# Kernel optimization log

Measured on AMD Instinct MI355X. Metric: run time of the kernel, lower is better.

Reference implementation:

```python
import jax, jax.numpy as jnp
import numpy as np

B, C, S, H, W = 2, 192, 16, 32, 32
NH, P = 6, 4          # num_heads, n_points (n_points hardcoded = 4 in source)
HD = C // NH          # head_dim = 32
HID = 4 * C           # mlp hidden (mlp_ratio = 4.0)
L = S * H * W
EPS = 1e-5


def _offset_bias():
    # Faithful to DeformAttention._reset_parameters grid init.
    thetas = np.arange(NH, dtype=np.float32) * (2.0 * np.pi / NH)
    g = np.stack([np.cos(thetas), np.sin(thetas) * np.cos(thetas), np.sin(thetas) * np.sin(thetas)], -1)
    g = g / np.abs(g).max(-1, keepdims=True)
    g = np.tile(g[:, None, :], (1, P, 1)).copy()
    for i in range(P):
        g[:, i, :] *= (i + 1)
    return jnp.asarray(g.reshape(-1), dtype=jnp.float32)


def setup_inputs() -> dict:
    key = jax.random.key(0)
    ks = jax.random.split(key, 8)
    w = lambda k, shp, s: jax.random.normal(k, shp, jnp.float32) * s
    return {
        "x": jax.random.normal(ks[0], (B, C, S, H, W), jnp.float32),
        "mask_matrix": 0,  # unused (shift_size == 0)
        "Wv": w(ks[1], (C, C), C ** -0.5), "bv": jnp.zeros((C,), jnp.float32),
        "Woff": w(ks[2], (C, NH * P * 3), 0.01), "boff": _offset_bias(),
        "Waw": w(ks[3], (C, NH * P), 0.02), "baw": jnp.zeros((NH * P,), jnp.float32),
        "Wout": w(ks[4], (C, C), C ** -0.5), "bout": jnp.zeros((C,), jnp.float32),
        "g2": jnp.ones((C,), jnp.float32), "b2": jnp.zeros((C,), jnp.float32),
        "W1": w(ks[5], (C, HID), C ** -0.5), "b1": jnp.zeros((HID,), jnp.float32),
        "W2": w(ks[6], (HID, C), HID ** -0.5), "b2m": jnp.zeros((C,), jnp.float32),
    }


def _layernorm(x, g, b):
    m = jnp.mean(x, -1, keepdims=True)
    v = jnp.mean(jnp.square(x - m), -1, keepdims=True)
    return (x - m) * jax.lax.rsqrt(v + EPS) * g + b


def _ref_points():
    # get_reference_points with valid_ratios == 1 (mask_ is all-zeros in source).
    d = (jnp.arange(S, dtype=jnp.float32) + 0.5) / S
    y = (jnp.arange(H, dtype=jnp.float32) + 0.5) / H
    x = (jnp.arange(W, dtype=jnp.float32) + 0.5) / W
    rd, ry, rx = jnp.meshgrid(d, y, x, indexing="ij")
    # stacked as (d, x, y), matching normalizer (D, W, H)
    return jnp.stack([rd.reshape(-1), rx.reshape(-1), ry.reshape(-1)], -1)  # (L, 3)


def _deform_core(value, loc, aw):
    # value: (B,L,NH,HD); loc: (B,L,NH,P,3) in [0,1] as (d,x,y); aw: (B,L,NH,P)
    v = value.transpose(0, 2, 1, 3)  # (B,NH,L,HD), L flattened as d*H*W + y*W + x
    pd = loc[..., 0] * S - 0.5  # align_corners=False pixel coords
    px = loc[..., 1] * W - 0.5
    py = loc[..., 2] * H - 0.5
    d0f, x0f, y0f = jnp.floor(pd), jnp.floor(px), jnp.floor(py)
    fd, fx, fy = pd - d0f, px - x0f, py - y0f
    d0, x0, y0 = d0f.astype(jnp.int32), x0f.astype(jnp.int32), y0f.astype(jnp.int32)
    acc = jnp.zeros((B, NH, L * P, HD), value.dtype)
    for dd in (0, 1):
        for dy in (0, 1):
            for dx in (0, 1):
                di, yi, xi = d0 + dd, y0 + dy, x0 + dx
                wgt = (fd if dd else 1.0 - fd) * (fy if dy else 1.0 - fy) * (fx if dx else 1.0 - fx)
                inb = (di >= 0) & (di < S) & (yi >= 0) & (yi < H) & (xi >= 0) & (xi < W)
                idx = (jnp.clip(di, 0, S - 1) * H + jnp.clip(yi, 0, H - 1)) * W + jnp.clip(xi, 0, W - 1)
                idx = idx.transpose(0, 2, 1, 3).reshape(B, NH, L * P)
                samp = jnp.take_along_axis(v, idx[..., None], axis=2)  # (B,NH,L*P,HD)
                wz = jnp.where(inb, wgt, 0.0).transpose(0, 2, 1, 3).reshape(B, NH, L * P, 1)
                acc = acc + samp * wz
    acc = acc.reshape(B, NH, L, P, HD)
    out = jnp.sum(acc * aw.transpose(0, 2, 1, 3)[..., None], axis=3)  # (B,NH,L,HD)
    return out.transpose(0, 2, 1, 3).reshape(B, L, NH * HD)


def reference(x, mask_matrix, Wv, bv, Woff, boff, Waw, baw, Wout, bout, g2, b2, W1, b1, W2, b2m):
    # shortcut = x.view(B, S*H*W, C) on channel-first memory (faithful to source view)
    shortcut = x.reshape(B, L, C)
    xp = x.transpose(0, 2, 3, 4, 1).reshape(B, L, C)  # token-major layout used by attn

    # DeformAttention
    value = (xp @ Wv + bv).reshape(B, L, NH, HD)
    off = (xp @ Woff + boff).reshape(B, L, NH, P, 3)
    aw = jax.nn.softmax((xp @ Waw + baw).reshape(B, L, NH, P), axis=-1)
    norm = jnp.array([S, W, H], jnp.float32)
    loc = _ref_points()[None, :, None, None, :] + off / norm  # (B,L,NH,P,3)
    attn = _deform_core(value, loc, aw) @ Wout + bout  # (B,L,C)

    h = shortcut + attn
    h = h + (jax.nn.gelu(_layernorm(h, g2, b2) @ W1 + b1, approximate=False) @ W2 + b2m)
    return h.reshape(B, S, H, W, C).transpose(0, 4, 1, 2, 3)  # (B,C,S,H,W)
```

## Files before the change

kernel.cpp:

```cpp
#include <hip/hip_runtime.h>
#include <hip/hip_bf16.h>
#include <math.h>

#define BB 2
#define CC 192
#define SS 16
#define HH 32
#define WW 32
#define NH 6
#define PP 4
#define HD 32
#define HID 768
#define LL (SS * HH * WW)
#define MTOK (BB * LL)
#define NPROJ 288

typedef unsigned short u16;
typedef u16 u16x8 __attribute__((ext_vector_type(8)));
typedef __bf16 bf16x8 __attribute__((ext_vector_type(8)));
typedef float f32x4 __attribute__((ext_vector_type(4)));

static __device__ __forceinline__ u16 f2b(float f) {
    __hip_bfloat16 h = __float2bfloat16(f);
    return *reinterpret_cast<u16*>(&h);
}

static __device__ __forceinline__ float fast_gelu(float v) {
    float z = 1.5957691216057308f * (v + 0.044715f * v * v * v);
    return v * __builtin_amdgcn_rcpf(1.0f + __expf(-z));
}

__global__ void build_weights(const float* __restrict__ Wv, const float* __restrict__ Woff,
                              const float* __restrict__ Waw, const float* __restrict__ Wout,
                              const float* __restrict__ W1, const float* __restrict__ W2,
                              const float* __restrict__ bv, const float* __restrict__ boff,
                              const float* __restrict__ baw,
                              u16* __restrict__ wcatT, u16* __restrict__ woutT,
                              u16* __restrict__ w1T, u16* __restrict__ w2T,
                              float* __restrict__ bcat) {
    int i = blockIdx.x * 256 + threadIdx.x;
    if (i < NPROJ * CC) {
        int n = i / CC, k = i % CC;
        float v = (n < 192) ? Wv[k * 192 + n]
                : (n < 264) ? Woff[k * 72 + (n - 192)]
                            : Waw[k * 24 + (n - 264)];
        wcatT[i] = f2b(v);
        return;
    }
    i -= NPROJ * CC;
    if (i < CC * CC) {
        int n = i / CC, k = i % CC;
        woutT[i] = f2b(Wout[k * CC + n]);
        return;
    }
    i -= CC * CC;
    if (i < HID * CC) {
        int n = i / CC, k = i % CC;
        w1T[i] = f2b(W1[k * HID + n]);
        return;
    }
    i -= HID * CC;
    if (i < CC * HID) {
        int n = i / HID, k = i % HID;
        w2T[i] = f2b(W2[k * CC + n]);
        return;
    }
    i -= CC * HID;
    if (i < NPROJ) {
        float v = (i < 192) ? bv[i] : (i < 264) ? boff[i - 192] : baw[i - 264];
        bcat[i] = v;
    }
}

__global__ void transpose_in(const float* __restrict__ x, u16* __restrict__ xp) {
    __shared__ float s[32][33];
    int b = blockIdx.z;
    int c0 = blockIdx.y * 32;
    int l0 = blockIdx.x * 32;
    int tx = threadIdx.x, ty = threadIdx.y;
#pragma unroll
    for (int r = 0; r < 32; r += 8)
        s[ty + r][tx] = x[((size_t)b * CC + c0 + ty + r) * LL + l0 + tx];
    __syncthreads();
#pragma unroll
    for (int r = 0; r < 32; r += 8)
        xp[((size_t)b * LL + l0 + ty + r) * CC + c0 + tx] = f2b(s[tx][ty + r]);
}

template<int EPI, int NF>
__global__ __launch_bounds__(256, 2) void gemm_mfma(const u16* __restrict__ A,
                                                    const u16* __restrict__ Bt,
                                                    const float* __restrict__ bias,
                                                    const float* __restrict__ add,
                                                    void* __restrict__ Cout,
                                                    void* __restrict__ Cout2,
                                                    int M, int N, int K) {
    constexpr int BN = NF * 32;
    constexpr int NB = (BN * 4 + 255) / 256;
    __shared__ u16 As[2][128][40];
    __shared__ u16 Bs[2][BN][40];
    int t = threadIdx.x;
    int m0 = blockIdx.y * 128;
    int n0 = blockIdx.x * BN;
    int w = t >> 6, lane = t & 63;
    int wm = w >> 1, wn = w & 1;
    int lrow = lane & 15, q = lane >> 4;
    int lk8 = q * 8;

    f32x4 acc[4][NF];
#pragma unroll
    for (int i = 0; i < 4; ++i)
#pragma unroll
        for (int f = 0; f < NF; ++f)
#pragma unroll
            for (int r = 0; r < 4; ++r) acc[i][f][r] = 0.f;

    int arow = t >> 2, aseg = (t & 3) * 8;
    const u16* Arow0 = A + (size_t)(m0 + arow) * K + aseg;
    const u16* Arow1 = A + (size_t)(m0 + arow + 64) * K + aseg;

    u16x8 av0, av1, bv[NB];
    av0 = *reinterpret_cast<const u16x8*>(Arow0);
    av1 = *reinterpret_cast<const u16x8*>(Arow1);
#pragma unroll
    for (int u2 = 0; u2 < NB; ++u2) {
        int ii = t + u2 * 256;
        if (ii < BN * 4) {
            int br = ii >> 2, bseg = (ii & 3) * 8;
            bv[u2] = *reinterpret_cast<const u16x8*>(Bt + (size_t)(n0 + br) * K + bseg);
        }
    }
    *reinterpret_cast<u16x8*>(&As[0][arow][aseg]) = av0;
    *reinterpret_cast<u16x8*>(&As[0][arow + 64][aseg]) = av1;
#pragma unroll
    for (int u2 = 0; u2 < NB; ++u2) {
        int ii = t + u2 * 256;
        if (ii < BN * 4) {
            int br = ii >> 2, bseg = (ii & 3) * 8;
            *reinterpret_cast<u16x8*>(&Bs[0][br][bseg]) = bv[u2];
        }
    }
    __syncthreads();

    int NT = K >> 5;
    int cur = 0;
    for (int ti = 0; ti < NT - 1; ++ti) {
        int k1 = (ti + 1) << 5;
        av0 = *reinterpret_cast<const u16x8*>(Arow0 + k1);
        av1 = *reinterpret_cast<const u16x8*>(Arow1 + k1);
#pragma unroll
        for (int u2 = 0; u2 < NB; ++u2) {
            int ii = t + u2 * 256;
            if (ii < BN * 4) {
                int br = ii >> 2, bseg = (ii & 3) * 8;
                bv[u2] = *reinterpret_cast<const u16x8*>(Bt + (size_t)(n0 + br) * K + k1 + bseg);
            }
        }
        {
            bf16x8 af[4], bfr[NF];
#pragma unroll
            for (int i = 0; i < 4; ++i)
                af[i] = *reinterpret_cast<const bf16x8*>(&As[cur][wm * 64 + i * 16 + lrow][lk8]);
#pragma unroll
            for (int f = 0; f < NF; ++f)
                bfr[f] = *reinterpret_cast<const bf16x8*>(&Bs[cur][wn * (16 * NF) + f * 16 + lrow][lk8]);
#pragma unroll
            for (int i = 0; i < 4; ++i)
#pragma unroll
                for (int f = 0; f < NF; ++f) {
                    if (EPI == 3)
                        acc[i][f] = __builtin_amdgcn_mfma_f32_16x16x32_bf16(af[i], bfr[f], acc[i][f], 0, 0, 0);
                    else
                        acc[i][f] = __builtin_amdgcn_mfma_f32_16x16x32_bf16(bfr[f], af[i], acc[i][f], 0, 0, 0);
                }
        }
        *reinterpret_cast<u16x8*>(&As[cur ^ 1][arow][aseg]) = av0;
        *reinterpret_cast<u16x8*>(&As[cur ^ 1][arow + 64][aseg]) = av1;
#pragma unroll
        for (int u2 = 0; u2 < NB; ++u2) {
            int ii = t + u2 * 256;
            if (ii < BN * 4) {
                int br = ii >> 2, bseg = (ii & 3) * 8;
                *reinterpret_cast<u16x8*>(&Bs[cur ^ 1][br][bseg]) = bv[u2];
            }
        }
        __syncthreads();
        cur ^= 1;
    }
    {
        bf16x8 af[4], bfr[NF];
#pragma unroll
        for (int i = 0; i < 4; ++i)
            af[i] = *reinterpret_cast<const bf16x8*>(&As[cur][wm * 64 + i * 16 + lrow][lk8]);
#pragma unroll
        for (int f = 0; f < NF; ++f)
            bfr[f] = *reinterpret_cast<const bf16x8*>(&Bs[cur][wn * (16 * NF) + f * 16 + lrow][lk8]);
#pragma unroll
        for (int i = 0; i < 4; ++i)
#pragma unroll
            for (int f = 0; f < NF; ++f) {
                if (EPI == 3)
                    acc[i][f] = __builtin_amdgcn_mfma_f32_16x16x32_bf16(af[i], bfr[f], acc[i][f], 0, 0, 0);
                else
                    acc[i][f] = __builtin_amdgcn_mfma_f32_16x16x32_bf16(bfr[f], af[i], acc[i][f], 0, 0, 0);
            }
    }

    if (EPI == 3) {
#pragma unroll
        for (int i = 0; i < 4; ++i) {
#pragma unroll
            for (int f = 0; f < NF; ++f) {
                int n = n0 + wn * (16 * NF) + f * 16 + lrow;
                float bvn = bias[n];
                int mb = m0 + wm * 64 + i * 16 + q * 4;
                float4 vv;
#pragma unroll
                for (int r = 0; r < 4; ++r)
                    ((float*)&vv)[r] = acc[i][f][r] + bvn + add[(size_t)(mb + r) * N + n];
                int b = mb >> 14, l = mb & (LL - 1);
                *reinterpret_cast<float4*>((float*)Cout + ((size_t)b * CC + n) * LL + l) = vv;
            }
        }
    } else {
#pragma unroll
        for (int i = 0; i < 4; ++i) {
            int m = m0 + wm * 64 + i * 16 + lrow;
#pragma unroll
            for (int f = 0; f < NF; ++f) {
                int nq = n0 + wn * (16 * NF) + f * 16 + q * 4;
                float4 bias4 = *reinterpret_cast<const float4*>(bias + nq);
                if (EPI == 0) {
                    if (nq < 192) {
                        int h = nq >> 5, hd = nq & 31;
                        int b = m >> 14, l = m & (LL - 1);
                        u16 p0 = f2b(acc[i][f][0] + bias4.x);
                        u16 p1 = f2b(acc[i][f][1] + bias4.y);
                        u16 p2 = f2b(acc[i][f][2] + bias4.z);
                        u16 p3 = f2b(acc[i][f][3] + bias4.w);
                        uint2 pk = make_uint2((unsigned)p0 | ((unsigned)p1 << 16),
                                              (unsigned)p2 | ((unsigned)p3 << 16));
                        *reinterpret_cast<uint2*>(
                            (u16*)Cout + (((size_t)b * NH + h) * LL + l) * HD + hd) = pk;
                    } else {
                        float4 vv;
                        vv.x = acc[i][f][0] + bias4.x;
                        vv.y = acc[i][f][1] + bias4.y;
                        vv.z = acc[i][f][2] + bias4.z;
                        vv.w = acc[i][f][3] + bias4.w;
                        *reinterpret_cast<float4*>((float*)Cout2 + (size_t)m * 96 + (nq - 192)) = vv;
                    }
                } else if (EPI == 1) {
                    float4 add4 = *reinterpret_cast<const float4*>(add + (size_t)m * N + nq);
                    float4 vv;
                    vv.x = acc[i][f][0] + bias4.x + add4.x;
                    vv.y = acc[i][f][1] + bias4.y + add4.y;
                    vv.z = acc[i][f][2] + bias4.z + add4.z;
                    vv.w = acc[i][f][3] + bias4.w + add4.w;
                    *reinterpret_cast<float4*>((float*)Cout + (size_t)m * N + nq) = vv;
                } else {
                    u16 p0 = f2b(fast_gelu(acc[i][f][0] + bias4.x));
                    u16 p1 = f2b(fast_gelu(acc[i][f][1] + bias4.y));
                    u16 p2 = f2b(fast_gelu(acc[i][f][2] + bias4.z));
                    u16 p3 = f2b(fast_gelu(acc[i][f][3] + bias4.w));
                    uint2 pk = make_uint2((unsigned)p0 | ((unsigned)p1 << 16),
                                          (unsigned)p2 | ((unsigned)p3 << 16));
                    *reinterpret_cast<uint2*>((u16*)Cout + (size_t)m * N + nq) = pk;
                }
            }
        }
    }
}

__global__ __launch_bounds__(256) void deform_kernel(const u16* __restrict__ vbuf,
                                                     const float* __restrict__ offaw,
                                                     u16* __restrict__ dout) {
    __shared__ uint2 cw[8][32];
    int gl = threadIdx.x >> 5;
    int g = blockIdx.x * 8 + gl;
    int j = threadIdx.x & 31;
    int h = g % NH;
    int tmp = g / NH;
    int l = tmp % LL;
    int b = tmp / LL;
    int d = l >> 10, rem = l & 1023, y = rem >> 5, xw = rem & 31;

    const float* oa = offaw + (size_t)(b * LL + l) * 96;
    int p = j >> 3, cor = j & 7;
    int dx = cor & 1, dy = (cor >> 1) & 1, dd = cor >> 2;

    float4 lg = *reinterpret_cast<const float4*>(oa + 72 + h * 4);
    float mx = fmaxf(fmaxf(lg.x, lg.y), fmaxf(lg.z, lg.w));
    float e0 = __expf(lg.x - mx), e1 = __expf(lg.y - mx);
    float e2 = __expf(lg.z - mx), e3 = __expf(lg.w - mx);
    float inv = __builtin_amdgcn_rcpf(e0 + e1 + e2 + e3);
    float ep = (p == 0) ? e0 : (p == 1) ? e1 : (p == 2) ? e2 : e3;
    float awp = ep * inv;

    const float* op = oa + (h * 4 + p) * 3;
    float pd = (d + 0.5f) + op[0] - 0.5f;
    float px = (xw + 0.5f) + op[1] - 0.5f;
    float py = (y + 0.5f) + op[2] - 0.5f;
    float d0f = floorf(pd), x0f = floorf(px), y0f = floorf(py);
    float fd = pd - d0f, fx = px - x0f, fy = py - y0f;
    int di = (int)d0f + dd, yi = (int)y0f + dy, xi = (int)x0f + dx;
    bool inb = (di >= 0) & (di < SS) & (yi >= 0) & (yi < HH) & (xi >= 0) & (xi < WW);
    float wgt = (dd ? fd : 1.f - fd) * (dy ? fy : 1.f - fy) * (dx ? fx : 1.f - fx) * awp;
    wgt = inb ? wgt : 0.f;
    int dic = min(max(di, 0), SS - 1);
    int yic = min(max(yi, 0), HH - 1);
    int xic = min(max(xi, 0), WW - 1);
    int bo = (((dic * HH) + yic) * WW + xic) * (HD * 2);

    cw[gl][j] = make_uint2((unsigned)bo, __float_as_uint(wgt));
    __syncthreads();

    int half = j >> 4, jc = j & 15;
    const char* vbase2 = (const char*)(vbuf + ((size_t)(b * NH + h) * LL) * HD) + 4 * jc;
    const uint4* cw4 = reinterpret_cast<const uint4*>(&cw[gl][half * 16]);
    float a0 = 0.f, a1 = 0.f;
#pragma unroll
    for (int qq = 0; qq < 8; ++qq) {
        uint4 c = cw4[qq];
        unsigned u0 = *reinterpret_cast<const unsigned*>(vbase2 + c.x);
        unsigned u1 = *reinterpret_cast<const unsigned*>(vbase2 + c.z);
        float w0 = __uint_as_float(c.y), w1 = __uint_as_float(c.w);
        a0 += w0 * __uint_as_float(u0 << 16);
        a1 += w0 * __uint_as_float(u0 & 0xffff0000u);
        a0 += w1 * __uint_as_float(u1 << 16);
        a1 += w1 * __uint_as_float(u1 & 0xffff0000u);
    }
    a0 += __shfl_xor(a0, 16);
    a1 += __shfl_xor(a1, 16);
    if (half == 0) {
        unsigned pk = (unsigned)f2b(a0) | ((unsigned)f2b(a1) << 16);
        *reinterpret_cast<unsigned*>(dout + (size_t)(b * LL + l) * CC + h * HD + 2 * jc) = pk;
    }
}

__global__ __launch_bounds__(256) void layernorm_kernel(const float* __restrict__ hin,
                                                        const float* __restrict__ g2,
                                                        const float* __restrict__ b2,
                                                        u16* __restrict__ lnout) {
    int row = blockIdx.x * 4 + (threadIdx.x >> 6);
    int lane = threadIdx.x & 63;
    const float* hr = hin + (size_t)row * CC;
    float v0 = hr[lane], v1 = hr[lane + 64], v2 = hr[lane + 128];
    float s = v0 + v1 + v2;
    float sq = v0 * v0 + v1 * v1 + v2 * v2;
#pragma unroll
    for (int o = 32; o > 0; o >>= 1) {
        s += __shfl_xor(s, o);
        sq += __shfl_xor(sq, o);
    }
    float m = s * (1.0f / CC);
    float var = sq * (1.0f / CC) - m * m;
    float r = rsqrtf(var + 1e-5f);
    u16* lo = lnout + (size_t)row * CC;
    lo[lane]       = f2b((v0 - m) * r * g2[lane]       + b2[lane]);
    lo[lane + 64]  = f2b((v1 - m) * r * g2[lane + 64]  + b2[lane + 64]);
    lo[lane + 128] = f2b((v2 - m) * r * g2[lane + 128] + b2[lane + 128]);
}

extern "C" void kernel_launch(void* const* d_in, const int* in_sizes, int n_in,
                              void* d_out, int out_size, void* d_ws, size_t ws_size,
                              hipStream_t stream) {
    const float* x    = (const float*)d_in[0];
    const float* Wv   = (const float*)d_in[2];
    const float* bv   = (const float*)d_in[3];
    const float* Woff = (const float*)d_in[4];
    const float* boff = (const float*)d_in[5];
    const float* Waw  = (const float*)d_in[6];
    const float* baw  = (const float*)d_in[7];
    const float* Wout = (const float*)d_in[8];
    const float* bout = (const float*)d_in[9];
    const float* g2   = (const float*)d_in[10];
    const float* b2   = (const float*)d_in[11];
    const float* W1   = (const float*)d_in[12];
    const float* b1   = (const float*)d_in[13];
    const float* W2   = (const float*)d_in[14];
    const float* b2m  = (const float*)d_in[15];

    char* wsb = (char*)d_ws;
    u16*   xp    = (u16*)(wsb + 0);
    u16*   vbuf  = (u16*)(wsb + 12582912);
    float* offaw = (float*)(wsb + 25165824);
    u16*   dbuf  = (u16*)(wsb + 0);
    u16*   hid   = (u16*)(wsb + 12582912);
    float* hbuf  = (float*)(wsb + 66060288);
    u16*   ln    = (u16*)(wsb + 92274688);
    u16*   wcatT = (u16*)(wsb + 105906176);
    u16*   woutT = wcatT + NPROJ * CC;
    u16*   w1T   = woutT + CC * CC;
    u16*   w2T   = w1T + HID * CC;
    float* bcat  = (float*)(w2T + CC * HID);
    float* out   = (float*)d_out;

    int wtot = NPROJ * CC + CC * CC + HID * CC + CC * HID + NPROJ;
    build_weights<<<(wtot + 255) / 256, 256, 0, stream>>>(
        Wv, Woff, Waw, Wout, W1, W2, bv, boff, baw, wcatT, woutT, w1T, w2T, bcat);
    transpose_in<<<dim3(LL / 32, CC / 32, BB), dim3(32, 8), 0, stream>>>(x, xp);
    gemm_mfma<0, 3><<<dim3(3, MTOK / 128), 256, 0, stream>>>(
        xp, wcatT, bcat, nullptr, vbuf, offaw, MTOK, NPROJ, CC);
    deform_kernel<<<(BB * LL * NH) / 8, 256, 0, stream>>>(vbuf, offaw, dbuf);
    gemm_mfma<1, 3><<<dim3(2, MTOK / 128), 256, 0, stream>>>(
        dbuf, woutT, bout, x , hbuf, nullptr, MTOK, CC, CC);
    layernorm_kernel<<<MTOK / 4, 256, 0, stream>>>(hbuf, g2, b2, ln);
    gemm_mfma<2, 6><<<dim3(4, MTOK / 128), 256, 0, stream>>>(
        ln, w1T, b1, nullptr, hid, nullptr, MTOK, HID, CC);
    gemm_mfma<3, 3><<<dim3(2, MTOK / 128), 256, 0, stream>>>(
        hid, w2T, b2m, hbuf, out, nullptr, MTOK, CC, HID);
}
```

Before: 228.0 us.

## Fuse LayerNorm into out-projection GEMM epilogue and softmax into projection GEMM

```diff
diff --git a/kernel.cpp b/kernel.cpp
--- a/kernel.cpp
+++ b/kernel.cpp
@@ -94,11 +94,15 @@
                                                     const float* __restrict__ add,
                                                     void* __restrict__ Cout,
                                                     void* __restrict__ Cout2,
+                                                    const float* __restrict__ g2p,
+                                                    const float* __restrict__ b2p,
                                                     int M, int N, int K) {
     constexpr int BN = NF * 32;
     constexpr int NB = (BN * 4 + 255) / 256;
     __shared__ u16 As[2][128][40];
     __shared__ u16 Bs[2][BN][40];
+    __shared__ float redS[2][2][64];
+    __shared__ float redQ[2][2][64];
     int t = threadIdx.x;
     int m0 = blockIdx.y * 128;
     int n0 = blockIdx.x * BN;
@@ -119,7 +123,7 @@
     const u16* Arow0 = A + (size_t)(m0 + arow) * K + aseg;
     const u16* Arow1 = A + (size_t)(m0 + arow + 64) * K + aseg;
 
-    u16x8 av0, av1, bv[NB];
+    u16x8 av0, av1, bvr[NB];
     av0 = *reinterpret_cast<const u16x8*>(Arow0);
     av1 = *reinterpret_cast<const u16x8*>(Arow1);
 #pragma unroll
@@ -127,7 +131,7 @@
         int ii = t + u2 * 256;
         if (ii < BN * 4) {
             int br = ii >> 2, bseg = (ii & 3) * 8;
-            bv[u2] = *reinterpret_cast<const u16x8*>(Bt + (size_t)(n0 + br) * K + bseg);
+            bvr[u2] = *reinterpret_cast<const u16x8*>(Bt + (size_t)(n0 + br) * K + bseg);
         }
     }
     *reinterpret_cast<u16x8*>(&As[0][arow][aseg]) = av0;
@@ -137,7 +141,7 @@
         int ii = t + u2 * 256;
         if (ii < BN * 4) {
             int br = ii >> 2, bseg = (ii & 3) * 8;
-            *reinterpret_cast<u16x8*>(&Bs[0][br][bseg]) = bv[u2];
+            *reinterpret_cast<u16x8*>(&Bs[0][br][bseg]) = bvr[u2];
         }
     }
     __syncthreads();
@@ -153,7 +157,7 @@
             int ii = t + u2 * 256;
             if (ii < BN * 4) {
                 int br = ii >> 2, bseg = (ii & 3) * 8;
-                bv[u2] = *reinterpret_cast<const u16x8*>(Bt + (size_t)(n0 + br) * K + k1 + bseg);
+                bvr[u2] = *reinterpret_cast<const u16x8*>(Bt + (size_t)(n0 + br) * K + k1 + bseg);
             }
         }
         {
@@ -181,7 +185,7 @@
             int ii = t + u2 * 256;
             if (ii < BN * 4) {
                 int br = ii >> 2, bseg = (ii & 3) * 8;
-                *reinterpret_cast<u16x8*>(&Bs[cur ^ 1][br][bseg]) = bv[u2];
+                *reinterpret_cast<u16x8*>(&Bs[cur ^ 1][br][bseg]) = bvr[u2];
             }
         }
         __syncthreads();
@@ -220,6 +224,59 @@
                     ((float*)&vv)[r] = acc[i][f][r] + bvn + add[(size_t)(mb + r) * N + n];
                 int b = mb >> 14, l = mb & (LL - 1);
                 *reinterpret_cast<float4*>((float*)Cout + ((size_t)b * CC + n) * LL + l) = vv;
+            }
+        }
+    } else if (EPI == 4) {
+        float s_[4], sq_[4];
+#pragma unroll
+        for (int i = 0; i < 4; ++i) {
+            int m = m0 + wm * 64 + i * 16 + lrow;
+            float s = 0.f, sq = 0.f;
+#pragma unroll
+            for (int f = 0; f < NF; ++f) {
+                int nq = n0 + wn * (16 * NF) + f * 16 + q * 4;
+                float4 bias4 = *reinterpret_cast<const float4*>(bias + nq);
+                float4 add4 = *reinterpret_cast<const float4*>(add + (size_t)m * N + nq);
+                float4 vv;
+#pragma unroll
+                for (int r = 0; r < 4; ++r) {
+                    float v = acc[i][f][r] + ((const float*)&bias4)[r] + ((const float*)&add4)[r];
+                    acc[i][f][r] = v;
+                    s += v;
+                    sq += v * v;
+                    ((float*)&vv)[r] = v;
+                }
+                *reinterpret_cast<float4*>((float*)Cout + (size_t)m * N + nq) = vv;
+            }
+            s += __shfl_xor(s, 16);  s += __shfl_xor(s, 32);
+            sq += __shfl_xor(sq, 16); sq += __shfl_xor(sq, 32);
+            s_[i] = s; sq_[i] = sq;
+        }
+        float wsel = (q == 0) ? s_[0] : (q == 1) ? s_[1] : (q == 2) ? s_[2] : s_[3];
+        float wqel = (q == 0) ? sq_[0] : (q == 1) ? sq_[1] : (q == 2) ? sq_[2] : sq_[3];
+        redS[wm][wn][q * 16 + lrow] = wsel;
+        redQ[wm][wn][q * 16 + lrow] = wqel;
+        __syncthreads();
+#pragma unroll
+        for (int i = 0; i < 4; ++i) {
+            int m = m0 + wm * 64 + i * 16 + lrow;
+            float ts = s_[i] + redS[wm][wn ^ 1][i * 16 + lrow];
+            float tq = sq_[i] + redQ[wm][wn ^ 1][i * 16 + lrow];
+            float mean = ts * (1.0f / CC);
+            float var = tq * (1.0f / CC) - mean * mean;
+            float rr = rsqrtf(var + 1e-5f);
+#pragma unroll
+            for (int f = 0; f < NF; ++f) {
+                int nq = n0 + wn * (16 * NF) + f * 16 + q * 4;
+                float4 gg = *reinterpret_cast<const float4*>(g2p + nq);
+                float4 bb = *reinterpret_cast<const float4*>(b2p + nq);
+                u16 p0 = f2b((acc[i][f][0] - mean) * rr * gg.x + bb.x);
+                u16 p1 = f2b((acc[i][f][1] - mean) * rr * gg.y + bb.y);
+                u16 p2 = f2b((acc[i][f][2] - mean) * rr * gg.z + bb.z);
+                u16 p3 = f2b((acc[i][f][3] - mean) * rr * gg.w + bb.w);
+                uint2 pk = make_uint2((unsigned)p0 | ((unsigned)p1 << 16),
+                                      (unsigned)p2 | ((unsigned)p3 << 16));
+                *reinterpret_cast<uint2*>((u16*)Cout2 + (size_t)m * CC + nq) = pk;
             }
         }
     } else {
@@ -242,22 +299,26 @@
                                               (unsigned)p2 | ((unsigned)p3 << 16));
                         *reinterpret_cast<uint2*>(
                             (u16*)Cout + (((size_t)b * NH + h) * LL + l) * HD + hd) = pk;
-                    } else {
+                    } else if (nq < 264) {
                         float4 vv;
                         vv.x = acc[i][f][0] + bias4.x;
                         vv.y = acc[i][f][1] + bias4.y;
                         vv.z = acc[i][f][2] + bias4.z;
                         vv.w = acc[i][f][3] + bias4.w;
                         *reinterpret_cast<float4*>((float*)Cout2 + (size_t)m * 96 + (nq - 192)) = vv;
+                    } else {
+                        float l0 = acc[i][f][0] + bias4.x;
+                        float l1 = acc[i][f][1] + bias4.y;
+                        float l2 = acc[i][f][2] + bias4.z;
+                        float l3 = acc[i][f][3] + bias4.w;
+                        float mx = fmaxf(fmaxf(l0, l1), fmaxf(l2, l3));
+                        float e0 = __expf(l0 - mx), e1 = __expf(l1 - mx);
+                        float e2 = __expf(l2 - mx), e3 = __expf(l3 - mx);
+                        float inv = __builtin_amdgcn_rcpf(e0 + e1 + e2 + e3);
+                        float4 vv;
+                        vv.x = e0 * inv; vv.y = e1 * inv; vv.z = e2 * inv; vv.w = e3 * inv;
+                        *reinterpret_cast<float4*>((float*)Cout2 + (size_t)m * 96 + (nq - 192)) = vv;
                     }
-                } else if (EPI == 1) {
-                    float4 add4 = *reinterpret_cast<const float4*>(add + (size_t)m * N + nq);
-                    float4 vv;
-                    vv.x = acc[i][f][0] + bias4.x + add4.x;
-                    vv.y = acc[i][f][1] + bias4.y + add4.y;
-                    vv.z = acc[i][f][2] + bias4.z + add4.z;
-                    vv.w = acc[i][f][3] + bias4.w + add4.w;
-                    *reinterpret_cast<float4*>((float*)Cout + (size_t)m * N + nq) = vv;
                 } else {
                     u16 p0 = f2b(fast_gelu(acc[i][f][0] + bias4.x));
                     u16 p1 = f2b(fast_gelu(acc[i][f][1] + bias4.y));
@@ -289,13 +350,7 @@
     int p = j >> 3, cor = j & 7;
     int dx = cor & 1, dy = (cor >> 1) & 1, dd = cor >> 2;
 
-    float4 lg = *reinterpret_cast<const float4*>(oa + 72 + h * 4);
-    float mx = fmaxf(fmaxf(lg.x, lg.y), fmaxf(lg.z, lg.w));
-    float e0 = __expf(lg.x - mx), e1 = __expf(lg.y - mx);
-    float e2 = __expf(lg.z - mx), e3 = __expf(lg.w - mx);
-    float inv = __builtin_amdgcn_rcpf(e0 + e1 + e2 + e3);
-    float ep = (p == 0) ? e0 : (p == 1) ? e1 : (p == 2) ? e2 : e3;
-    float awp = ep * inv;
+    float awp = oa[72 + h * 4 + p];
 
     const float* op = oa + (h * 4 + p) * 3;
     float pd = (d + 0.5f) + op[0] - 0.5f;
@@ -336,30 +391,6 @@
         unsigned pk = (unsigned)f2b(a0) | ((unsigned)f2b(a1) << 16);
         *reinterpret_cast<unsigned*>(dout + (size_t)(b * LL + l) * CC + h * HD + 2 * jc) = pk;
     }
-}
-
-__global__ __launch_bounds__(256) void layernorm_kernel(const float* __restrict__ hin,
-                                                        const float* __restrict__ g2,
-                                                        const float* __restrict__ b2,
-                                                        u16* __restrict__ lnout) {
-    int row = blockIdx.x * 4 + (threadIdx.x >> 6);
-    int lane = threadIdx.x & 63;
-    const float* hr = hin + (size_t)row * CC;
-    float v0 = hr[lane], v1 = hr[lane + 64], v2 = hr[lane + 128];
-    float s = v0 + v1 + v2;
-    float sq = v0 * v0 + v1 * v1 + v2 * v2;
-#pragma unroll
-    for (int o = 32; o > 0; o >>= 1) {
-        s += __shfl_xor(s, o);
-        sq += __shfl_xor(sq, o);
-    }
-    float m = s * (1.0f / CC);
-    float var = sq * (1.0f / CC) - m * m;
-    float r = rsqrtf(var + 1e-5f);
-    u16* lo = lnout + (size_t)row * CC;
-    lo[lane]       = f2b((v0 - m) * r * g2[lane]       + b2[lane]);
-    lo[lane + 64]  = f2b((v1 - m) * r * g2[lane + 64]  + b2[lane + 64]);
-    lo[lane + 128] = f2b((v2 - m) * r * g2[lane + 128] + b2[lane + 128]);
 }
 
 extern "C" void kernel_launch(void* const* d_in, const int* in_sizes, int n_in,
@@ -401,13 +432,12 @@
         Wv, Woff, Waw, Wout, W1, W2, bv, boff, baw, wcatT, woutT, w1T, w2T, bcat);
     transpose_in<<<dim3(LL / 32, CC / 32, BB), dim3(32, 8), 0, stream>>>(x, xp);
     gemm_mfma<0, 3><<<dim3(3, MTOK / 128), 256, 0, stream>>>(
-        xp, wcatT, bcat, nullptr, vbuf, offaw, MTOK, NPROJ, CC);
+        xp, wcatT, bcat, nullptr, vbuf, offaw, nullptr, nullptr, MTOK, NPROJ, CC);
     deform_kernel<<<(BB * LL * NH) / 8, 256, 0, stream>>>(vbuf, offaw, dbuf);
-    gemm_mfma<1, 3><<<dim3(2, MTOK / 128), 256, 0, stream>>>(
-        dbuf, woutT, bout, x , hbuf, nullptr, MTOK, CC, CC);
-    layernorm_kernel<<<MTOK / 4, 256, 0, stream>>>(hbuf, g2, b2, ln);
+    gemm_mfma<4, 6><<<dim3(1, MTOK / 128), 256, 0, stream>>>(
+        dbuf, woutT, bout, x , hbuf, ln, g2, b2, MTOK, CC, CC);
     gemm_mfma<2, 6><<<dim3(4, MTOK / 128), 256, 0, stream>>>(
-        ln, w1T, b1, nullptr, hid, nullptr, MTOK, HID, CC);
+        ln, w1T, b1, nullptr, hid, nullptr, nullptr, nullptr, MTOK, HID, CC);
     gemm_mfma<3, 3><<<dim3(2, MTOK / 128), 256, 0, stream>>>(
-        hid, w2T, b2m, hbuf, out, nullptr, MTOK, CC, HID);
-}
+        hid, w2T, b2m, hbuf, out, nullptr, nullptr, nullptr, MTOK, CC, HID);
+}
```

Measured after the change: 221.4 us. 1.03x faster.
